# Kernel tuning notes

Hardware: AMD Instinct MI355X
Metric: run time of the kernel (lower is better)

The kernel has to match this reference:

```python
import jax, jax.numpy as jnp
import numpy as np

IN_FEATURES = 512
NUM_CENTERS = 2048
BATCH = 16384


def setup_inputs() -> dict:
    key = jax.random.key(0)
    kx, kc = jax.random.split(key)
    x = jax.random.normal(kx, (BATCH, IN_FEATURES), dtype=jnp.float32)
    centers = jax.random.normal(kc, (NUM_CENTERS, IN_FEATURES), dtype=jnp.float32)
    beta = jnp.ones((NUM_CENTERS,), dtype=jnp.float32)
    return {"x": x, "centers": centers, "beta": beta}


def reference(x, centers, beta):
    x_sq = jnp.sum(x * x, axis=-1, keepdims=True)            # (B, 1)
    c_sq = jnp.sum(centers * centers, axis=-1)                # (M,)
    cross = jnp.einsum('bd,md->bm', x, centers)               # (B, M)
    dist_sq = x_sq + c_sq[None, :] - 2.0 * cross              # (B, M)
    return jnp.exp(-beta[None, :] * dist_sq)
```

## Files before the change

kernel.cpp:

```cpp
#include <hip/hip_runtime.h>
#include <stdint.h>

#define IN_F   512
#define N_CTR  2048
#define BATCH  16384

#define BM 128
#define BN 128
#define BK 64
#define NKT (IN_F / BK)

using bf16x8  = __attribute__((ext_vector_type(8))) short;
using f32x4   = __attribute__((ext_vector_type(4))) float;
using ushort8 = __attribute__((ext_vector_type(8))) unsigned short;

typedef const __attribute__((address_space(1))) void* gptr_t;
typedef __attribute__((address_space(3))) void* lptr_t;

static __device__ __forceinline__ unsigned short f2bf(float f) {
    uint32_t u = __builtin_bit_cast(uint32_t, f);
    uint32_t r = u + 0x7fffu + ((u >> 16) & 1u);
    return (unsigned short)(r >> 16);
}

__global__ void convert_all(const float* __restrict__ x,
                            const float* __restrict__ c,
                            unsigned short* __restrict__ xb,
                            unsigned short* __restrict__ cb,
                            float* __restrict__ xsq,
                            float* __restrict__ csq) {
    const int wave = threadIdx.x >> 6;
    const int lane = threadIdx.x & 63;
    const int row  = blockIdx.x * 4 + wave;

    const float* src;
    unsigned short* dst;
    float* sq;
    int r;
    if (row < BATCH) { src = x; dst = xb; sq = xsq; r = row; }
    else             { src = c; dst = cb; sq = csq; r = row - BATCH; }

    const float* rp = src + (size_t)r * IN_F + lane * 8;
    float4 a = *reinterpret_cast<const float4*>(rp);
    float4 b = *reinterpret_cast<const float4*>(rp + 4);
    float ss = a.x*a.x + a.y*a.y + a.z*a.z + a.w*a.w
             + b.x*b.x + b.y*b.y + b.z*b.z + b.w*b.w;
    ushort8 o;
    o[0]=f2bf(a.x); o[1]=f2bf(a.y); o[2]=f2bf(a.z); o[3]=f2bf(a.w);
    o[4]=f2bf(b.x); o[5]=f2bf(b.y); o[6]=f2bf(b.z); o[7]=f2bf(b.w);
    *reinterpret_cast<ushort8*>(dst + (size_t)r * IN_F + lane * 8) = o;
    #pragma unroll
    for (int off = 32; off > 0; off >>= 1) ss += __shfl_down(ss, off);
    if (lane == 0) sq[r] = ss;
}

__launch_bounds__(256, 3)
__global__ void rbf_gemm(const unsigned short* __restrict__ xb,
                         const unsigned short* __restrict__ cb,
                         const float* __restrict__ xsq,
                         const float* __restrict__ csq,
                         const float* __restrict__ beta,
                         float* __restrict__ out) {
    __shared__ unsigned short As[BM * BK];
    __shared__ unsigned short Bs[BN * BK];

    const int tid  = threadIdx.x;
    const int wid  = tid >> 6;
    const int lane = tid & 63;
    const int wr   = wid >> 1;
    const int wc   = wid & 1;

    const int nwg = gridDim.x;
    const int bid = blockIdx.x;
    const int swz = (bid & 7) * (nwg >> 3) + (bid >> 3);

    const int ntn = N_CTR / BN;
    const int tm  = swz / ntn;
    const int tn  = swz % ntn;

    const int srow = (wid * 4) * 8 + (lane >> 3);
    const int scol = (lane & 7) * 8;
    const unsigned short* gA0 = xb + (size_t)(tm * BM + srow) * IN_F + scol;
    const unsigned short* gB0 = cb + (size_t)(tn * BN + srow) * IN_F + scol;

    f32x4 acc[4][4] = {};

    for (int kt = 0; kt < NKT; ++kt) {
        const int kbase = kt * BK;
        #pragma unroll
        for (int i = 0; i < 4; ++i) {
            const unsigned short* ga = gA0 + (size_t)(i * 8) * IN_F + kbase;
            const unsigned short* gb = gB0 + (size_t)(i * 8) * IN_F + kbase;
            __builtin_amdgcn_global_load_lds((gptr_t)ga, (lptr_t)(As + (wid * 4 + i) * 512), 16, 0, 0);
            __builtin_amdgcn_global_load_lds((gptr_t)gb, (lptr_t)(Bs + (wid * 4 + i) * 512), 16, 0, 0);
        }
        __syncthreads();

        #pragma unroll
        for (int kk = 0; kk < 2; ++kk) {
            bf16x8 af[4], bfr[4];
            const int kreg = kk * 32 + (lane >> 4) * 8;
            #pragma unroll
            for (int mi = 0; mi < 4; ++mi)
                af[mi] = *reinterpret_cast<const bf16x8*>(
                    &As[(wr * 64 + mi * 16 + (lane & 15)) * BK + kreg]);
            #pragma unroll
            for (int ni = 0; ni < 4; ++ni)
                bfr[ni] = *reinterpret_cast<const bf16x8*>(
                    &Bs[(wc * 64 + ni * 16 + (lane & 15)) * BK + kreg]);
            #pragma unroll
            for (int mi = 0; mi < 4; ++mi)
                #pragma unroll
                for (int ni = 0; ni < 4; ++ni)
                    acc[mi][ni] = __builtin_amdgcn_mfma_f32_16x16x32_bf16(
                        af[mi], bfr[ni], acc[mi][ni], 0, 0, 0);
        }
        __syncthreads();
    }

    const int row0 = tm * BM + wr * 64;
    const int col0 = tn * BN + wc * 64;
    #pragma unroll
    for (int ni = 0; ni < 4; ++ni) {
        const int col = col0 + ni * 16 + (lane & 15);
        const float bt = beta[col];
        const float cs = csq[col];
        #pragma unroll
        for (int mi = 0; mi < 4; ++mi) {
            #pragma unroll
            for (int j = 0; j < 4; ++j) {
                const int row = row0 + mi * 16 + (lane >> 4) * 4 + j;
                const float d = xsq[row] + cs - 2.0f * acc[mi][ni][j];
                out[(size_t)row * N_CTR + col] = __expf(-bt * d);
            }
        }
    }
}

__global__ void rbf_naive(const float* __restrict__ x,
                          const float* __restrict__ c,
                          const float* __restrict__ beta,
                          float* __restrict__ out) {
    __shared__ float xs[IN_F];
    const int row = blockIdx.x;
    const int col = blockIdx.y * 128 + threadIdx.x;
    for (int i = threadIdx.x; i < IN_F; i += 128)
        xs[i] = x[(size_t)row * IN_F + i];
    __syncthreads();
    const float* cp = c + (size_t)col * IN_F;
    float d = 0.f;
    #pragma unroll 4
    for (int k = 0; k < IN_F; k += 4) {
        float4 cv = *reinterpret_cast<const float4*>(cp + k);
        float t0 = xs[k + 0] - cv.x;
        float t1 = xs[k + 1] - cv.y;
        float t2 = xs[k + 2] - cv.z;
        float t3 = xs[k + 3] - cv.w;
        d += t0 * t0 + t1 * t1 + t2 * t2 + t3 * t3;
    }
    out[(size_t)row * N_CTR + col] = __expf(-beta[col] * d);
}

extern "C" void kernel_launch(void* const* d_in, const int* in_sizes, int n_in,
                              void* d_out, int out_size, void* d_ws, size_t ws_size,
                              hipStream_t stream) {
    const float* x    = (const float*)d_in[0];
    const float* c    = (const float*)d_in[1];
    const float* beta = (const float*)d_in[2];
    float* out        = (float*)d_out;

    const size_t need = (size_t)BATCH * IN_F * 2 + (size_t)N_CTR * IN_F * 2
                      + (size_t)BATCH * 4 + (size_t)N_CTR * 4;
    if (ws_size >= need) {
        unsigned short* xbuf = (unsigned short*)d_ws;
        unsigned short* cbuf = xbuf + (size_t)BATCH * IN_F;
        float* xsq = (float*)(cbuf + (size_t)N_CTR * IN_F);
        float* csq = xsq + BATCH;
        convert_all<<<(BATCH + N_CTR) / 4, 256, 0, stream>>>(x, c, xbuf, cbuf, xsq, csq);
        rbf_gemm<<<(BATCH / BM) * (N_CTR / BN), 256, 0, stream>>>(
            xbuf, cbuf, xsq, csq, beta, out);
    } else {
        rbf_naive<<<dim3(BATCH, N_CTR / 128), 128, 0, stream>>>(x, c, beta, out);
    }
}
```

Baseline: 73.54 us.

## Use 256x256 tiles with double-buffered swizzled LDS and 8-wave phased pipeline

The GEMM tile grows from 128x128 to 256x256 and runs with 512 threads (8 waves). LDS is double-buffered and split into halves, so the next k-tile's global-to-LDS loads are issued while the current one is computed in four barrier-separated phases. LDS columns are XOR-swizzled to avoid bank conflicts, and s_setprio raises priority around the MFMA blocks. The goal is to hide load latency and raise arithmetic intensity, at the cost of more registers, fewer workgroups (512), and fragile hand-written waitcnt and barrier ordering.

After: 68.34 us. -7.1%, faster.

```diff
diff --git a/kernel.cpp b/kernel.cpp
--- a/kernel.cpp
+++ b/kernel.cpp
@@ -5,10 +5,10 @@
 #define N_CTR  2048
 #define BATCH  16384
 
-#define BM 128
-#define BN 128
+#define BM 256
+#define BN 256
 #define BK 64
-#define NKT (IN_F / BK)
+#define NT (IN_F / BK)
 
 using bf16x8  = __attribute__((ext_vector_type(8))) short;
 using f32x4   = __attribute__((ext_vector_type(4))) float;
@@ -54,83 +54,116 @@
     if (lane == 0) sq[r] = ss;
 }
 
-__launch_bounds__(256, 3)
+__launch_bounds__(512, 2)
 __global__ void rbf_gemm(const unsigned short* __restrict__ xb,
                          const unsigned short* __restrict__ cb,
                          const float* __restrict__ xsq,
                          const float* __restrict__ csq,
                          const float* __restrict__ beta,
                          float* __restrict__ out) {
-    __shared__ unsigned short As[BM * BK];
-    __shared__ unsigned short Bs[BN * BK];
+    __shared__ __align__(16) unsigned short lds[2][2][2][128 * 64];
 
     const int tid  = threadIdx.x;
     const int wid  = tid >> 6;
     const int lane = tid & 63;
-    const int wr   = wid >> 1;
-    const int wc   = wid & 1;
-
-    const int nwg = gridDim.x;
+    const int wr   = wid >> 2;
+    const int wc   = wid & 3;
+
     const int bid = blockIdx.x;
-    const int swz = (bid & 7) * (nwg >> 3) + (bid >> 3);
-
+    const int swz = (bid & 7) * 64 + (bid >> 3);
     const int ntn = N_CTR / BN;
     const int tm  = swz / ntn;
     const int tn  = swz % ntn;
 
-    const int srow = (wid * 4) * 8 + (lane >> 3);
-    const int scol = (lane & 7) * 8;
-    const unsigned short* gA0 = xb + (size_t)(tm * BM + srow) * IN_F + scol;
-    const unsigned short* gB0 = cb + (size_t)(tn * BN + srow) * IN_F + scol;
-
-    f32x4 acc[4][4] = {};
-
-    for (int kt = 0; kt < NKT; ++kt) {
-        const int kbase = kt * BK;
-        #pragma unroll
-        for (int i = 0; i < 4; ++i) {
-            const unsigned short* ga = gA0 + (size_t)(i * 8) * IN_F + kbase;
-            const unsigned short* gb = gB0 + (size_t)(i * 8) * IN_F + kbase;
-            __builtin_amdgcn_global_load_lds((gptr_t)ga, (lptr_t)(As + (wid * 4 + i) * 512), 16, 0, 0);
-            __builtin_amdgcn_global_load_lds((gptr_t)gb, (lptr_t)(Bs + (wid * 4 + i) * 512), 16, 0, 0);
-        }
-        __syncthreads();
-
+    const int csrc = (lane & 7) ^ ((lane >> 3) & 7);
+
+    f32x4 acc[8][4] = {};
+
+    auto stage_half = [&](int buf, int op, int h, int kt) {
+        const unsigned short* src = (op == 0) ? xb : cb;
+        const int tb = ((op == 0) ? tm : tn) * 256;
+        #pragma unroll
+        for (int j = 0; j < 2; ++j) {
+            const int rl = wid * 16 + j * 8 + (lane >> 3);
+            const unsigned short* g = src + (size_t)(tb + h * 128 + rl) * IN_F
+                                      + kt * BK + csrc * 8;
+            __builtin_amdgcn_global_load_lds(
+                (gptr_t)g, (lptr_t)&lds[buf][op][h][(wid * 16 + j * 8) * 64],
+                16, 0, 0);
+        }
+    };
+
+    bf16x8 af[4][2];
+    bf16x8 bfv[2][2];
+
+    auto phase_compute = [&](int buf, int mh, int nh) {
         #pragma unroll
         for (int kk = 0; kk < 2; ++kk) {
-            bf16x8 af[4], bfr[4];
-            const int kreg = kk * 32 + (lane >> 4) * 8;
+            const int coff = (((kk * 4 + (lane >> 4)) ^ (lane & 7)) * 8);
+            if (nh == 0) {
+                #pragma unroll
+                for (int i = 0; i < 4; ++i) {
+                    const int rl = (mh * 4 + i) * 16 + (lane & 15);
+                    af[i][kk] = *reinterpret_cast<const bf16x8*>(
+                        &lds[buf][0][wr][rl * 64 + coff]);
+                }
+            }
             #pragma unroll
-            for (int mi = 0; mi < 4; ++mi)
-                af[mi] = *reinterpret_cast<const bf16x8*>(
-                    &As[(wr * 64 + mi * 16 + (lane & 15)) * BK + kreg]);
+            for (int j = 0; j < 2; ++j) {
+                const int rl = (wc & 1) * 64 + (nh * 2 + j) * 16 + (lane & 15);
+                bfv[j][kk] = *reinterpret_cast<const bf16x8*>(
+                    &lds[buf][1][wc >> 1][rl * 64 + coff]);
+            }
+        }
+        __builtin_amdgcn_s_setprio(1);
+        #pragma unroll
+        for (int i = 0; i < 4; ++i)
             #pragma unroll
-            for (int ni = 0; ni < 4; ++ni)
-                bfr[ni] = *reinterpret_cast<const bf16x8*>(
-                    &Bs[(wc * 64 + ni * 16 + (lane & 15)) * BK + kreg]);
-            #pragma unroll
-            for (int mi = 0; mi < 4; ++mi)
+            for (int j = 0; j < 2; ++j)
                 #pragma unroll
-                for (int ni = 0; ni < 4; ++ni)
-                    acc[mi][ni] = __builtin_amdgcn_mfma_f32_16x16x32_bf16(
-                        af[mi], bfr[ni], acc[mi][ni], 0, 0, 0);
-        }
-        __syncthreads();
-    }
-
-    const int row0 = tm * BM + wr * 64;
-    const int col0 = tn * BN + wc * 64;
-    #pragma unroll
-    for (int ni = 0; ni < 4; ++ni) {
-        const int col = col0 + ni * 16 + (lane & 15);
+                for (int kk = 0; kk < 2; ++kk)
+                    acc[mh * 4 + i][nh * 2 + j] =
+                        __builtin_amdgcn_mfma_f32_16x16x32_bf16(
+                            af[i][kk], bfv[j][kk], acc[mh * 4 + i][nh * 2 + j],
+                            0, 0, 0);
+        __builtin_amdgcn_s_setprio(0);
+    };
+
+    #pragma unroll
+    for (int p = 0; p < 4; ++p) stage_half(0, p >> 1, p & 1, 0);
+
+    #pragma unroll
+    for (int t = 0; t < NT; ++t) {
+        const int cur = t & 1;
+        const int nxt = cur ^ 1;
+        const int ktn = (t + 1 < NT) ? t + 1 : NT - 1;
+        #pragma unroll
+        for (int p = 0; p < 4; ++p) {
+            stage_half(nxt, p >> 1, p & 1, ktn);
+            if (p == 0)
+                asm volatile("s_waitcnt vmcnt(2)" ::: "memory");
+            asm volatile("s_barrier" ::: "memory");
+            __builtin_amdgcn_sched_barrier(0);
+            phase_compute(cur, p >> 1, p & 1);
+            __builtin_amdgcn_sched_barrier(0);
+            asm volatile("s_barrier" ::: "memory");
+        }
+    }
+    asm volatile("s_waitcnt vmcnt(0)" ::: "memory");
+
+    const int row0 = tm * 256 + wr * 128;
+    const int col0 = tn * 256 + wc * 64;
+    #pragma unroll
+    for (int n = 0; n < 4; ++n) {
+        const int col = col0 + n * 16 + (lane & 15);
         const float bt = beta[col];
         const float cs = csq[col];
         #pragma unroll
-        for (int mi = 0; mi < 4; ++mi) {
+        for (int m = 0; m < 8; ++m) {
             #pragma unroll
             for (int j = 0; j < 4; ++j) {
-                const int row = row0 + mi * 16 + (lane >> 4) * 4 + j;
-                const float d = xsq[row] + cs - 2.0f * acc[mi][ni][j];
+                const int row = row0 + m * 16 + (lane >> 4) * 4 + j;
+                const float d = xsq[row] + cs - 2.0f * acc[m][n][j];
                 out[(size_t)row * N_CTR + col] = __expf(-bt * d);
             }
         }
@@ -177,7 +210,7 @@
         float* xsq = (float*)(cbuf + (size_t)N_CTR * IN_F);
         float* csq = xsq + BATCH;
         convert_all<<<(BATCH + N_CTR) / 4, 256, 0, stream>>>(x, c, xbuf, cbuf, xsq, csq);
-        rbf_gemm<<<(BATCH / BM) * (N_CTR / BN), 256, 0, stream>>>(
+        rbf_gemm<<<(BATCH / BM) * (N_CTR / BN), 512, 0, stream>>>(
             xbuf, cbuf, xsq, csq, beta, out);
     } else {
         rbf_naive<<<dim3(BATCH, N_CTR / 128), 128, 0, stream>>>(x, c, beta, out);
```

## Keep full-K center tile in LDS and stream A fragments from global

Applied to the files above, without the earlier changes.

Replaces the 128x128 k-tiled GEMM with 256x64 tiles and 512 threads. The whole 64x512 bf16 center slice is loaded once into XOR-swizzled LDS. Each wave then streams its x rows straight from global into registers with double buffering, which removes the per-k-step barriers and the LDS staging of A. This trades LDS reuse of x for more global traffic: each x row is now read by 32 column tiles instead of 16. It also relies on the cache to absorb those repeated reads, and uses 64KB of LDS per block, which limits occupancy.

Result: slower. 90.75 us (+23.4%).

```diff
diff --git a/kernel.cpp b/kernel.cpp
--- a/kernel.cpp
+++ b/kernel.cpp
@@ -4,11 +4,11 @@
 #define IN_F   512
 #define N_CTR  2048
 #define BATCH  16384
+#define BK     64
+#define NKT    (IN_F / BK)
 
-#define BM 128
-#define BN 128
-#define BK 64
-#define NKT (IN_F / BK)
+#define BM 256
+#define BN 64
 
 using bf16x8  = __attribute__((ext_vector_type(8))) short;
 using f32x4   = __attribute__((ext_vector_type(4))) float;
@@ -54,85 +54,97 @@
     if (lane == 0) sq[r] = ss;
 }
 
-__launch_bounds__(256, 3)
-__global__ void rbf_gemm(const unsigned short* __restrict__ xb,
-                         const unsigned short* __restrict__ cb,
-                         const float* __restrict__ xsq,
-                         const float* __restrict__ csq,
-                         const float* __restrict__ beta,
-                         float* __restrict__ out) {
-    __shared__ unsigned short As[BM * BK];
-    __shared__ unsigned short Bs[BN * BK];
+__launch_bounds__(512)
+__global__ void rbf_gemm_stream(const unsigned short* __restrict__ xb,
+                                const unsigned short* __restrict__ cb,
+                                const float* __restrict__ xsq,
+                                const float* __restrict__ csq,
+                                const float* __restrict__ beta,
+                                float* __restrict__ out) {
+    __shared__ __align__(16) unsigned short Bs[BN * IN_F];
 
     const int tid  = threadIdx.x;
     const int wid  = tid >> 6;
     const int lane = tid & 63;
-    const int wr   = wid >> 1;
-    const int wc   = wid & 1;
+    const int g16  = lane >> 4;
+    const int l16  = lane & 15;
 
-    const int nwg = gridDim.x;
-    const int bid = blockIdx.x;
-    const int swz = (bid & 7) * (nwg >> 3) + (bid >> 3);
+    const int bid  = blockIdx.x;
+    const int swzc = (bid & 7) * 256 + (bid >> 3);
+    const int tm   = swzc >> 5;
+    const int tn   = swzc & 31;
 
-    const int ntn = N_CTR / BN;
-    const int tm  = swz / ntn;
-    const int tn  = swz % ntn;
+    #pragma unroll
+    for (int rr = 0; rr < 8; ++rr) {
+        const int r = wid * 8 + rr;
+        const unsigned short* src = cb + (size_t)(tn * BN + r) * IN_F + (lane ^ rr) * 8;
+        __builtin_amdgcn_global_load_lds((gptr_t)src, (lptr_t)(Bs + r * IN_F), 16, 0, 0);
+    }
 
-    const int srow = (wid * 4) * 8 + (lane >> 3);
-    const int scol = (lane & 7) * 8;
-    const unsigned short* gA0 = xb + (size_t)(tm * BM + srow) * IN_F + scol;
-    const unsigned short* gB0 = cb + (size_t)(tn * BN + srow) * IN_F + scol;
+    const int arow0 = tm * BM + wid * 32;
+    const unsigned short* gA = xb + (size_t)(arow0 + l16) * IN_F + g16 * 8;
 
-    f32x4 acc[4][4] = {};
+    f32x4  acc[2][4] = {};
+    bf16x8 afA[2][2], afB[2][2];
 
-    for (int kt = 0; kt < NKT; ++kt) {
-        const int kbase = kt * BK;
+    auto loadA = [&](bf16x8 dst[2][2], int kt) {
         #pragma unroll
-        for (int i = 0; i < 4; ++i) {
-            const unsigned short* ga = gA0 + (size_t)(i * 8) * IN_F + kbase;
-            const unsigned short* gb = gB0 + (size_t)(i * 8) * IN_F + kbase;
-            __builtin_amdgcn_global_load_lds((gptr_t)ga, (lptr_t)(As + (wid * 4 + i) * 512), 16, 0, 0);
-            __builtin_amdgcn_global_load_lds((gptr_t)gb, (lptr_t)(Bs + (wid * 4 + i) * 512), 16, 0, 0);
-        }
-        __syncthreads();
+        for (int i = 0; i < 2; ++i)
+            #pragma unroll
+            for (int kk = 0; kk < 2; ++kk)
+                dst[i][kk] = *reinterpret_cast<const bf16x8*>(
+                    gA + (size_t)(i * 16) * IN_F + kt * BK + kk * 32);
+    };
 
+    auto computeKT = [&](bf16x8 af[2][2], int kt) {
         #pragma unroll
         for (int kk = 0; kk < 2; ++kk) {
-            bf16x8 af[4], bfr[4];
-            const int kreg = kk * 32 + (lane >> 4) * 8;
+            bf16x8 bfr[4];
             #pragma unroll
-            for (int mi = 0; mi < 4; ++mi)
-                af[mi] = *reinterpret_cast<const bf16x8*>(
-                    &As[(wr * 64 + mi * 16 + (lane & 15)) * BK + kreg]);
+            for (int ni = 0; ni < 4; ++ni) {
+                const int rb   = ni * 16 + l16;
+                const int slot = kt * 8 + ((kk * 4 + g16) ^ (rb & 7));
+                bfr[ni] = *reinterpret_cast<const bf16x8*>(
+                    (const char*)Bs + rb * (IN_F * 2) + slot * 16);
+            }
+            #pragma unroll
+            for (int i = 0; i < 2; ++i)
+                #pragma unroll
+                for (int ni = 0; ni < 4; ++ni)
+                    acc[i][ni] = __builtin_amdgcn_mfma_f32_16x16x32_bf16(
+                        af[i][kk], bfr[ni], acc[i][ni], 0, 0, 0);
+        }
+    };
+
+    loadA(afA, 0);
+    __syncthreads();
+
+    #pragma unroll 1
+    for (int kt = 0; kt < NKT; kt += 2) {
+        loadA(afB, kt + 1);
+        computeKT(afA, kt);
+        if (kt + 2 < NKT) loadA(afA, kt + 2);
+        computeKT(afB, kt + 1);
+    }
+
+    const int colb = tn * BN;
+    float csb[4], btb[4];
+    #pragma unroll
+    for (int ni = 0; ni < 4; ++ni) {
+        const int col = colb + ni * 16 + l16;
+        csb[ni] = csq[col];
+        btb[ni] = beta[col];
+    }
+    #pragma unroll
+    for (int i = 0; i < 2; ++i) {
+        #pragma unroll
+        for (int j = 0; j < 4; ++j) {
+            const int row = arow0 + i * 16 + g16 * 4 + j;
+            const float xs = xsq[row];
+            float* op = out + (size_t)row * N_CTR + colb;
             #pragma unroll
             for (int ni = 0; ni < 4; ++ni)
-                bfr[ni] = *reinterpret_cast<const bf16x8*>(
-                    &Bs[(wc * 64 + ni * 16 + (lane & 15)) * BK + kreg]);
-            #pragma unroll
-            for (int mi = 0; mi < 4; ++mi)
-                #pragma unroll
-                for (int ni = 0; ni < 4; ++ni)
-                    acc[mi][ni] = __builtin_amdgcn_mfma_f32_16x16x32_bf16(
-                        af[mi], bfr[ni], acc[mi][ni], 0, 0, 0);
-        }
-        __syncthreads();
-    }
-
-    const int row0 = tm * BM + wr * 64;
-    const int col0 = tn * BN + wc * 64;
-    #pragma unroll
-    for (int ni = 0; ni < 4; ++ni) {
-        const int col = col0 + ni * 16 + (lane & 15);
-        const float bt = beta[col];
-        const float cs = csq[col];
-        #pragma unroll
-        for (int mi = 0; mi < 4; ++mi) {
-            #pragma unroll
-            for (int j = 0; j < 4; ++j) {
-                const int row = row0 + mi * 16 + (lane >> 4) * 4 + j;
-                const float d = xsq[row] + cs - 2.0f * acc[mi][ni][j];
-                out[(size_t)row * N_CTR + col] = __expf(-bt * d);
-            }
+                op[ni * 16 + l16] = __expf(-btb[ni] * (xs + csb[ni] - 2.0f * acc[i][ni][j]));
         }
     }
 }
@@ -177,7 +189,7 @@
         float* xsq = (float*)(cbuf + (size_t)N_CTR * IN_F);
         float* csq = xsq + BATCH;
         convert_all<<<(BATCH + N_CTR) / 4, 256, 0, stream>>>(x, c, xbuf, cbuf, xsq, csq);
-        rbf_gemm<<<(BATCH / BM) * (N_CTR / BN), 256, 0, stream>>>(
+        rbf_gemm_stream<<<(BATCH / BM) * (N_CTR / BN), 512, 0, stream>>>(
             xbuf, cbuf, xsq, csq, beta, out);
     } else {
         rbf_naive<<<dim3(BATCH, N_CTR / 128), 128, 0, stream>>>(x, c, beta, out);
```
